# Kernel tuning notes

Measured on AMD Instinct MI355X. Metric: run time of the kernel, lower is better.

The kernel has to match this reference:

```python
import jax, jax.numpy as jnp
import numpy as np
from jax.ops import segment_sum, segment_max

B = 512          # parcels (batch of graphs)
P = 200          # poi nodes per parcel
N = B * P        # total poi nodes
E_POI = N * 16   # intra-parcel poi graph edges
HID = 256
IN_CH = 64
HEADS = 3
OUT = 12
T0 = 0.9
SLOPE = 0.2      # GATConv leaky_relu negative slope
NODE_GRAPH = jnp.arange(N, dtype=jnp.int32) // P  # poi node -> parcel id
ARANGE_N = jnp.arange(N, dtype=jnp.int32)


def setup_inputs() -> dict:
    key = jax.random.key(0)
    ks = jax.random.split(key, 24)
    g = lambda i, shape: jax.random.normal(ks[i], shape, jnp.float32) * 0.05
    # poi graph edges constrained within each parcel block
    src0 = jax.random.randint(ks[0], (E_POI,), 0, N, dtype=jnp.int32)
    off = jax.random.randint(ks[1], (E_POI,), 0, P, dtype=jnp.int32)
    return dict(
        g_poi_features=jax.random.normal(ks[2], (N, IN_CH), jnp.float32),
        img_feat=jax.random.normal(ks[3], (B, 2048), jnp.float32),
        edge_src=src0,
        edge_dst=(src0 // P) * P + off,
        W_gcn1=g(4, (IN_CH, HID)), b_gcn1=jnp.zeros((HID,), jnp.float32),
        W_gcn2=g(5, (HID, HID)), b_gcn2=jnp.zeros((HID,), jnp.float32),
        W_hrs=g(6, (2048, HID)), b_hrs=jnp.zeros((HID,), jnp.float32),
        W_proj_hrs=g(7, (HID, HID)), b_proj_hrs=jnp.zeros((HID,), jnp.float32),
        W_proj_poi=g(8, (HID, HID)), b_proj_poi=jnp.zeros((HID,), jnp.float32),
        W_gat_in=g(9, (HID, HEADS * HID)), al_in=g(10, (HEADS, HID)), ar_in=g(11, (HEADS, HID)),
        W_gat_with=g(12, (HID, HEADS * HID)), al_with=g(13, (HEADS, HID)), ar_with=g(14, (HEADS, HID)),
        W_hrsgnn=g(15, (HID, HID)),
        W_poignn=g(16, (HID, HID)),
        W_fc=g(17, (4 * HID, OUT)), b_fc=jnp.zeros((OUT,), jnp.float32),
    )


def _gcn(x, src, dst, W, b):
    # DGL GraphConv, norm='both', self-loops added
    s = jnp.concatenate([src, ARANGE_N])
    d = jnp.concatenate([dst, ARANGE_N])
    deg = segment_sum(jnp.ones_like(s, jnp.float32), d, num_segments=N)
    norm = jax.lax.rsqrt(jnp.maximum(deg, 1.0))
    h = (x @ W) * norm[:, None]
    m = segment_sum(h[s], d, num_segments=N)
    return m * norm[:, None] + b


def _gat(h_src, h_dst, src, dst, n_dst, W, al, ar):
    # DGL GATConv math: shared fc, additive attention, edge-softmax over dst
    fs = (h_src @ W).reshape(-1, HEADS, HID)
    fd = (h_dst @ W).reshape(-1, HEADS, HID)
    el = (fs * al).sum(-1)   # [n_src, H]
    er = (fd * ar).sum(-1)   # [n_dst, H]
    e = el[src] + er[dst]
    e = jnp.where(e > 0, e, SLOPE * e)
    m = segment_max(e, dst, num_segments=n_dst)
    w = jnp.exp(e - m[dst])
    z = segment_sum(w, dst, num_segments=n_dst)
    alpha = w / (z[dst] + 1e-9)
    out = segment_sum(fs[src] * alpha[:, :, None], dst, num_segments=n_dst)
    return out.mean(1)  # mean over heads (parcel_output.mean(1) in source)


def _mean_nodes(x):
    # dgl.mean_nodes over uniform-size batched graphs
    return segment_sum(x, NODE_GRAPH, num_segments=B) / P


def reference(g_poi_features, img_feat, edge_src, edge_dst,
              W_gcn1, b_gcn1, W_gcn2, b_gcn2, W_hrs, b_hrs,
              W_proj_hrs, b_proj_hrs, W_proj_poi, b_proj_poi,
              W_gat_in, al_in, ar_in, W_gat_with, al_with, ar_with,
              W_hrsgnn, W_poignn, W_fc, b_fc):
    # hrs_encoder: ResNet50 backbone modeled as precomputed 2048-d feats + replaced fc
    hrs = img_feat @ W_hrs + b_hrs                                  # [B, HID]
    # poi_encoder: 2-layer GCN over batched poi graph
    x = jax.nn.relu(_gcn(g_poi_features, edge_src, edge_dst, W_gcn1, b_gcn1))
    poi_nodes = _gcn(x, edge_src, edge_dst, W_gcn2, b_gcn2)         # [N, HID]
    poi_pooled = _mean_nodes(poi_nodes)                             # [B, HID]
    # mid-level fused similarity
    med = jnp.concatenate([hrs, poi_pooled], axis=1)
    med = med / jnp.linalg.norm(med, axis=1, keepdims=True)
    med_output = (med @ med.T + 1.0) / 2.0                          # [B, B]
    # UniSimGraph: GCN on thresholded parcel-similarity graph
    adj = jnp.where(med_output >= T0, 1.0, 0.0)
    adj = jnp.maximum(adj, jnp.eye(B, dtype=jnp.float32))
    dinv = jax.lax.rsqrt(adj.sum(1))
    nadj = adj * dinv[:, None] * dinv[None, :]
    hrs_agg = jax.nn.relu(nadj @ (hrs @ W_hrsgnn))                  # [B, HID]
    poi_agg = jax.nn.relu(nadj @ (poi_pooled @ W_poignn))           # [B, HID]
    # getHetGraph: bipartite poi<->parcel GAT, 3 heads, sum-aggregate, head-mean
    ph = hrs @ W_proj_hrs + b_proj_hrs                              # parcel feats
    pp = poi_nodes @ W_proj_poi + b_proj_poi                        # poi feats
    poi2img = _gat(pp, ph, ARANGE_N, NODE_GRAPH, B, W_gat_in, al_in, ar_in)      # [B, HID]
    img2poi = _gat(ph, pp, NODE_GRAPH, ARANGE_N, N, W_gat_with, al_with, ar_with)  # [N, HID]
    img2poi_pooled = _mean_nodes(img2poi)                           # [B, HID]
    # MutualAgg concat order: [img2poi, poi2poi(=poi_agg), poi2img, img2img(=hrs_agg)]
    agg = jnp.concatenate([img2poi_pooled, poi_agg, poi2img, hrs_agg], axis=1)
    output = agg @ W_fc + b_fc                                      # [B, OUT]
    return (output, med_output)
```

## Files before the change

kernel.cpp:

```cpp
#include <hip/hip_runtime.h>
#include <hip/hip_bf16.h>
#include <math.h>


#define N_NODES 102400
#define B_PAR   512
#define P_NODES 200
#define E_EDGES 1638400
#define HIDF    256

typedef __attribute__((ext_vector_type(8))) short bf16x8;
typedef __attribute__((ext_vector_type(4))) float f32x4;

__device__ __forceinline__ unsigned short f2bf(float x) {
    unsigned u = __builtin_bit_cast(unsigned, x);
    u += 0x7fffu + ((u >> 16) & 1u);
    return (unsigned short)(u >> 16);
}
__device__ __forceinline__ float bf2f(unsigned short h) {
    return __builtin_bit_cast(float, (unsigned)h << 16);
}
__device__ __forceinline__ int lds_off(int row, int kbyte) {
    return row * 128 + ((((kbyte >> 4) ^ (row & 7)) << 4) | (kbyte & 15));
}
template<bool BF16SRC>
__device__ __forceinline__ bf16x8 load_row8(const void* p, size_t elemoff) {
    if constexpr (BF16SRC) {
        return *(const bf16x8*)((const unsigned short*)p + elemoff);
    } else {
        const float* ap = (const float*)p + elemoff;
        float4 lo = *(const float4*)ap;
        float4 hi = *(const float4*)(ap + 4);
        union { bf16x8 v; unsigned short u[8]; } pk;
        pk.u[0] = f2bf(lo.x); pk.u[1] = f2bf(lo.y);
        pk.u[2] = f2bf(lo.z); pk.u[3] = f2bf(lo.w);
        pk.u[4] = f2bf(hi.x); pk.u[5] = f2bf(hi.y);
        pk.u[6] = f2bf(hi.z); pk.u[7] = f2bf(hi.w);
        return pk.v;
    }
}
__device__ __forceinline__ bf16x8 u8x8_to_bf16(uint2 w) {
    union { bf16x8 v; unsigned short u[8]; } r;
#pragma unroll
    for (int b = 0; b < 4; ++b) {
        r.u[b]     = (unsigned short)(__builtin_bit_cast(unsigned,
                        (float)((w.x >> (8 * b)) & 255u)) >> 16);
        r.u[4 + b] = (unsigned short)(__builtin_bit_cast(unsigned,
                        (float)((w.y >> (8 * b)) & 255u)) >> 16);
    }
    return r.v;
}
__device__ __forceinline__ unsigned long long pack4bf(f32x4 v) {
    union { unsigned long long u; unsigned short h[4]; } pk;
    pk.h[0] = f2bf(v[0]); pk.h[1] = f2bf(v[1]);
    pk.h[2] = f2bf(v[2]); pk.h[3] = f2bf(v[3]);
    return pk.u;
}

__global__ __launch_bounds__(512, 2) void gcnA_k(
    const unsigned char* __restrict__ Adj, const float* __restrict__ gp,
    const float* __restrict__ nrm, const unsigned short* __restrict__ W1t,
    const float* __restrict__ b1, unsigned short* __restrict__ X1nT)
{
    __shared__ unsigned char XnU[32768];
    __shared__ unsigned char AXU[32768];

    const int tid  = threadIdx.x;
    const int p    = blockIdx.x;
    const int lane = tid & 63;
    const int wave = tid >> 6;
    const int frow = lane & 15;
    const int fq   = lane >> 4;
    const int r4   = fq << 2;
    const f32x4 fz = {0.f, 0.f, 0.f, 0.f};

    uint2 adjr[2][7];
#pragma unroll
    for (int mi = 0; mi < 2; ++mi) {
        const unsigned char* ar = Adj + ((size_t)p << 16)
            + (size_t)(wave * 32 + mi * 16 + frow) * 256 + fq * 8;
#pragma unroll
        for (int ks = 0; ks < 7; ++ks)
            adjr[mi][ks] = *(const uint2*)(ar + ks * 32);
    }
    bf16x8 w1f[2][2];
#pragma unroll
    for (int mi = 0; mi < 2; ++mi)
#pragma unroll
        for (int ks = 0; ks < 2; ++ks)
            w1f[mi][ks] = *(const bf16x8*)(W1t
                + (size_t)(wave * 32 + mi * 16 + frow) * 64 + ks * 32 + fq * 8);

    for (int gi = wave; gi < 28; gi += 8) {
        int s0 = gi * 8;
        union { bf16x8 v; unsigned short h[8]; } pk;
#pragma unroll
        for (int t = 0; t < 8; ++t) {
            int s = s0 + t;
            float val = 0.f;
            if (s < 200)
                val = gp[((size_t)(p * 200 + s)) * 64 + lane] * nrm[p * 200 + s];
            pk.h[t] = f2bf(val);
        }
        *(bf16x8*)(XnU + lds_off((s0 >> 6) * 64 + lane, (s0 & 63) * 2)) = pk.v;
    }
    __syncthreads();

#pragma unroll
    for (int mi_d = 0; mi_d < 2; ++mi_d) {
        bf16x8 adjf[7];
#pragma unroll
        for (int ks = 0; ks < 7; ++ks) adjf[ks] = u8x8_to_bf16(adjr[mi_d][ks]);
#pragma unroll
        for (int kt = 0; kt < 4; ++kt) {
            f32x4 a2 = fz;
#pragma unroll
            for (int ks = 0; ks < 7; ++ks) {
                bf16x8 af = *(const bf16x8*)(XnU + lds_off(
                    (ks >> 1) * 64 + kt * 16 + frow, ((ks & 1) * 32 + fq * 8) * 2));
                a2 = __builtin_amdgcn_mfma_f32_16x16x32_bf16(af, adjf[ks], a2, 0, 0, 0);
            }
            *(unsigned long long*)(AXU + lds_off(
                wave * 32 + mi_d * 16 + frow, kt * 32 + fq * 8)) = pack4bf(a2);
        }
    }
    __syncthreads();

    f32x4 acc3[2][16];
#pragma unroll
    for (int i = 0; i < 2; ++i)
#pragma unroll
        for (int j = 0; j < 16; ++j) acc3[i][j] = fz;
#pragma unroll
    for (int ks = 0; ks < 2; ++ks)
#pragma unroll
        for (int ni = 0; ni < 16; ++ni) {
            bf16x8 bfr = *(const bf16x8*)(AXU + lds_off(
                ni * 16 + frow, ks * 64 + fq * 16));
            acc3[0][ni] = __builtin_amdgcn_mfma_f32_16x16x32_bf16(w1f[0][ks], bfr, acc3[0][ni], 0, 0, 0);
            acc3[1][ni] = __builtin_amdgcn_mfma_f32_16x16x32_bf16(w1f[1][ks], bfr, acc3[1][ni], 0, 0, 0);
        }

    float nrd[16];
#pragma unroll
    for (int ni = 0; ni < 16; ++ni) {
        int d = ni * 16 + frow;
        nrd[ni] = (d < 200) ? nrm[p * 200 + d] : 0.f;
    }
#pragma unroll
    for (int mi = 0; mi < 2; ++mi)
#pragma unroll
        for (int j = 0; j < 4; ++j) {
            int f = wave * 32 + mi * 16 + r4 + j;
            float bv = b1[f];
#pragma unroll
            for (int ni = 0; ni < 16; ++ni) {
                int d = ni * 16 + frow;
                if (d < 224) {
                    float v = fmaxf(acc3[mi][ni][j] * nrd[ni] + bv, 0.f) * nrd[ni];
                    X1nT[((size_t)p * 256 + f) * 224 + d] = f2bf(v);
                }
            }
        }
}

__global__ __launch_bounds__(512, 2) void gcnBG_k(
    const unsigned char* __restrict__ Adj, const unsigned short* __restrict__ X1nT,
    const unsigned short* __restrict__ W2t, const float* __restrict__ nrm,
    const float* __restrict__ b2, const float* __restrict__ er,
    const float* __restrict__ wu, float* __restrict__ qout,
    float* __restrict__ pool, unsigned short* __restrict__ poolb)
{
    __shared__ unsigned char BbU[2][16384];
    __shared__ unsigned char AXbU[16384];
    __shared__ unsigned char W2bU[16384];
    __shared__ float wush[768];
    __shared__ float esh[600];
    __shared__ float qsh[1024];
    __shared__ float mz[8];

    const int tid  = threadIdx.x;
    const int p    = blockIdx.x;
    const int lane = tid & 63;
    const int wave = tid >> 6;
    const int frow = lane & 15;
    const int fq   = lane >> 4;
    const int r4   = fq << 2;
    const f32x4 fz = {0.f, 0.f, 0.f, 0.f};

    bf16x8 adjb[2][7];
#pragma unroll
    for (int mi = 0; mi < 2; ++mi) {
        const unsigned char* ar = Adj + ((size_t)p << 16)
            + (size_t)(wave * 32 + mi * 16 + frow) * 256 + fq * 8;
#pragma unroll
        for (int ks = 0; ks < 7; ++ks)
            adjb[mi][ks] = u8x8_to_bf16(*(const uint2*)(ar + ks * 32));
    }

    for (int i = tid; i < 768; i += 512) wush[i] = wu[i];
    for (int i = tid; i < 1024; i += 512) qsh[i] = 0.f;

    f32x4 acc5[2][16];
#pragma unroll
    for (int i = 0; i < 2; ++i)
#pragma unroll
        for (int j = 0; j < 16; ++j) acc5[i][j] = fz;

    auto bbDst = [&](unsigned char* base, int idx) {
        int fl = idx / 28, soct = idx - fl * 28;
        int s0 = soct * 8;
        return base + lds_off((s0 >> 6) * 32 + fl, (s0 & 63) * 2);
    };
    auto bbSrc = [&](int c, int idx) {
        int fl = idx / 28, soct = idx - fl * 28;
        return (const uint4*)(X1nT + ((size_t)p * 256 + c * 32 + fl) * 224 + soct * 8);
    };
    auto w2Dst = [&](int idx) {
        int f = idx >> 2, oct = idx & 3;
        return W2bU + lds_off(f >> 1, (f & 1) * 64 + oct * 16);
    };

    {
        *(uint4*)bbDst(BbU[0], tid) = *bbSrc(0, tid);
        if (tid < 384) *(uint4*)bbDst(BbU[0], tid + 512) = *bbSrc(0, tid + 512);
#pragma unroll
        for (int i = 0; i < 2; ++i) {
            int idx = tid + i * 512;
            int f = idx >> 2, oct = idx & 3;
            *(uint4*)w2Dst(idx) = *(const uint4*)(W2t + (size_t)f * 256 + oct * 8);
        }
    }
    __syncthreads();

    uint4 stw[2];
    for (int c = 0; c < 8; ++c) {
        if (c > 0) {
#pragma unroll
            for (int i = 0; i < 2; ++i)
                *(uint4*)w2Dst(tid + i * 512) = stw[i];
        }
        uint4 stb0, stb1;
        if (c < 7) {
            stb0 = *bbSrc(c + 1, tid);
            if (tid < 384) stb1 = *bbSrc(c + 1, tid + 512);
#pragma unroll
            for (int i = 0; i < 2; ++i) {
                int idx = tid + i * 512;
                int f = idx >> 2, oct = idx & 3;
                stw[i] = *(const uint4*)(W2t + (size_t)f * 256 + (c + 1) * 32 + oct * 8);
            }
        }
        const unsigned char* Bc = BbU[c & 1];
        f32x4 acc4[2][2];
#pragma unroll
        for (int i = 0; i < 2; ++i)
#pragma unroll
            for (int j = 0; j < 2; ++j) acc4[i][j] = fz;
#pragma unroll
        for (int ks = 0; ks < 7; ++ks) {
#pragma unroll
            for (int mi_f = 0; mi_f < 2; ++mi_f) {
                bf16x8 af = *(const bf16x8*)(Bc + lds_off(
                    (ks >> 1) * 32 + mi_f * 16 + frow, ((ks & 1) * 32 + fq * 8) * 2));
                acc4[0][mi_f] = __builtin_amdgcn_mfma_f32_16x16x32_bf16(af, adjb[0][ks], acc4[0][mi_f], 0, 0, 0);
                acc4[1][mi_f] = __builtin_amdgcn_mfma_f32_16x16x32_bf16(af, adjb[1][ks], acc4[1][mi_f], 0, 0, 0);
            }
        }
#pragma unroll
        for (int mi_d = 0; mi_d < 2; ++mi_d)
#pragma unroll
            for (int mi_f = 0; mi_f < 2; ++mi_f)
                *(unsigned long long*)(AXbU + lds_off(
                    wave * 16 + mi_d * 8 + (frow >> 1),
                    (frow & 1) * 64 + mi_f * 32 + fq * 8))
                    = pack4bf(acc4[mi_d][mi_f]);
        __syncthreads();
        bf16x8 a5[2];
        a5[0] = *(const bf16x8*)(AXbU + lds_off(
            wave * 16 + (frow >> 1), (frow & 1) * 64 + fq * 16));
        a5[1] = *(const bf16x8*)(AXbU + lds_off(
            wave * 16 + 8 + (frow >> 1), (frow & 1) * 64 + fq * 16));
#pragma unroll
        for (int ni = 0; ni < 16; ++ni) {
            bf16x8 bfr = *(const bf16x8*)(W2bU + lds_off(
                ni * 8 + (frow >> 1), (frow & 1) * 64 + fq * 16));
            acc5[0][ni] = __builtin_amdgcn_mfma_f32_16x16x32_bf16(a5[0], bfr, acc5[0][ni], 0, 0, 0);
            acc5[1][ni] = __builtin_amdgcn_mfma_f32_16x16x32_bf16(a5[1], bfr, acc5[1][ni], 0, 0, 0);
        }
        if (c < 7) {
            *(uint4*)bbDst(BbU[(c + 1) & 1], tid) = stb0;
            if (tid < 384) *(uint4*)bbDst(BbU[(c + 1) & 1], tid + 512) = stb1;
        }
        __syncthreads();
    }

    float b2v[16], nrv[2][4];
#pragma unroll
    for (int ni = 0; ni < 16; ++ni) b2v[ni] = b2[ni * 16 + frow];
#pragma unroll
    for (int mi = 0; mi < 2; ++mi)
#pragma unroll
        for (int j = 0; j < 4; ++j) {
            int d = wave * 32 + mi * 16 + r4 + j;
            nrv[mi][j] = (d < 200) ? nrm[p * 200 + d] : 0.f;
        }
    float er3[3];
#pragma unroll
    for (int h = 0; h < 3; ++h) er3[h] = er[p * 3 + h];

#pragma unroll
    for (int mi = 0; mi < 2; ++mi)
#pragma unroll
        for (int j = 0; j < 4; ++j) {
            float e0 = 0.f, e1 = 0.f, e2 = 0.f;
            float nr = nrv[mi][j];
#pragma unroll
            for (int ni = 0; ni < 16; ++ni) {
                float vv = acc5[mi][ni][j] * nr + b2v[ni];
                int wb = (ni * 16 + frow) * 3;
                e0 += vv * wush[wb];
                e1 += vv * wush[wb + 1];
                e2 += vv * wush[wb + 2];
            }
#pragma unroll
            for (int o = 1; o < 16; o <<= 1) {
                e0 += __shfl_xor(e0, o);
                e1 += __shfl_xor(e1, o);
                e2 += __shfl_xor(e2, o);
            }
            int d = wave * 32 + mi * 16 + r4 + j;
            if (frow == 0 && d < 200) {
                float t0 = e0 + er3[0]; t0 = t0 > 0.f ? t0 : 0.2f * t0;
                float t1 = e1 + er3[1]; t1 = t1 > 0.f ? t1 : 0.2f * t1;
                float t2 = e2 + er3[2]; t2 = t2 > 0.f ? t2 : 0.2f * t2;
                esh[d * 3 + 0] = t0;
                esh[d * 3 + 1] = t1;
                esh[d * 3 + 2] = t2;
            }
        }
    __syncthreads();

    if (wave < 3) {
        float mx = -1e30f;
        for (int n = lane; n < 200; n += 64) mx = fmaxf(mx, esh[n * 3 + wave]);
#pragma unroll
        for (int o = 32; o > 0; o >>= 1) mx = fmaxf(mx, __shfl_xor(mx, o));
        float sm = 0.f;
        for (int n = lane; n < 200; n += 64) sm += expf(esh[n * 3 + wave] - mx);
#pragma unroll
        for (int o = 32; o > 0; o >>= 1) sm += __shfl_xor(sm, o);
        if (lane == 0) { mz[wave] = mx; mz[4 + wave] = sm; }
    }
    __syncthreads();

    float alph[2][4][3];
#pragma unroll
    for (int mi = 0; mi < 2; ++mi)
#pragma unroll
        for (int j = 0; j < 4; ++j) {
            int d = wave * 32 + mi * 16 + r4 + j;
#pragma unroll
            for (int h = 0; h < 3; ++h)
                alph[mi][j][h] = (d < 200)
                    ? expf(esh[d * 3 + h] - mz[h]) / (mz[4 + h] + 1e-9f) : 0.f;
        }

#pragma unroll
    for (int cfn = 0; cfn < 4; ++cfn) {
        float qacc[16];
#pragma unroll
        for (int ni = 0; ni < 16; ++ni) qacc[ni] = 0.f;
        float csum = 0.f;
#pragma unroll
        for (int mi = 0; mi < 2; ++mi)
#pragma unroll
            for (int j = 0; j < 4; ++j) {
                int d = wave * 32 + mi * 16 + r4 + j;
                float coef = 0.f;
                if (d < 200) coef = (cfn < 3) ? alph[mi][j][cfn] : 0.005f;
                float cn = coef * nrv[mi][j];
                csum += coef;
#pragma unroll
                for (int ni = 0; ni < 16; ++ni)
                    qacc[ni] += cn * acc5[mi][ni][j];
            }
#pragma unroll
        for (int ni = 0; ni < 16; ++ni) {
            float v = qacc[ni] + csum * b2v[ni];
            v += __shfl_xor(v, 16);
            v += __shfl_xor(v, 32);
            if (fq == 0) atomicAdd(&qsh[cfn * 256 + ni * 16 + frow], v);
        }
    }
    __syncthreads();

    for (int i = tid; i < 1024; i += 512) {
        int cfn = i >> 8, f = i & 255;
        float s = qsh[i];
        if (cfn < 3) {
            qout[(size_t)p * 768 + i] = s;
        } else {
            pool[(size_t)p * 256 + f] = s;
            poolb[(size_t)p * 256 + f] = f2bf(s);
        }
    }
}

template<bool ABF16, bool BBF16, int OMODE, bool BIASF, bool RELUF,
         bool MEDOUT, int KCHUNK>
__global__ __launch_bounds__(256) void mm64_k(
    const void* __restrict__ Ain, const void* __restrict__ Bin,
    void* __restrict__ Cout, int M, int Nc, int K,
    const float* __restrict__ bias, float alpha)
{
    __shared__ bf16x8 smem_v[1024];
    unsigned char* Asm = (unsigned char*)smem_v;
    unsigned char* Bsm = Asm + 8192;

    const int tid  = threadIdx.x;
    const int m0   = blockIdx.y * 64;
    const int n0   = blockIdx.x * 64;
    const int sr   = tid >> 3, sc = tid & 7;
    const int lane = tid & 63;
    const int wm   = (tid >> 7) & 1, wn = (tid >> 6) & 1;
    const int frow = lane & 15;
    const int fko  = (lane >> 4) << 4;

    int kbeg = 0, kend = K;
    float* Cf = (float*)Cout;
    if (KCHUNK > 0) {
        kbeg = blockIdx.z * KCHUNK; kend = kbeg + KCHUNK;
        Cf += (size_t)blockIdx.z * M * Nc;
    }

    f32x4 acc[2][2];
    const f32x4 fz = {0.f, 0.f, 0.f, 0.f};
#pragma unroll
    for (int i = 0; i < 2; ++i)
#pragma unroll
        for (int j = 0; j < 2; ++j) acc[i][j] = fz;

    bf16x8 areg[2], breg[2];
    auto load_tiles = [&](int k0) {
#pragma unroll
        for (int i = 0; i < 2; ++i) {
            int row = sr + 32 * i;
            areg[i] = load_row8<ABF16>(Ain, (size_t)(m0 + row) * K + k0 + sc * 8);
            breg[i] = load_row8<BBF16>(Bin, (size_t)(n0 + row) * K + k0 + sc * 8);
        }
    };

    load_tiles(kbeg);
    for (int k0 = kbeg; k0 < kend; k0 += 64) {
        __syncthreads();
#pragma unroll
        for (int i = 0; i < 2; ++i) {
            *(bf16x8*)(Asm + lds_off(sr + 32 * i, sc * 16)) = areg[i];
            *(bf16x8*)(Bsm + lds_off(sr + 32 * i, sc * 16)) = breg[i];
        }
        __syncthreads();
        if (k0 + 64 < kend) load_tiles(k0 + 64);
#pragma unroll
        for (int ks = 0; ks < 2; ++ks) {
            const int kb = ks * 64 + fko;
            bf16x8 af[2], bfr[2];
#pragma unroll
            for (int t = 0; t < 2; ++t)
                af[t] = *(const bf16x8*)(Asm + lds_off(wm * 32 + t * 16 + frow, kb));
#pragma unroll
            for (int t = 0; t < 2; ++t)
                bfr[t] = *(const bf16x8*)(Bsm + lds_off(wn * 32 + t * 16 + frow, kb));
#pragma unroll
            for (int mi = 0; mi < 2; ++mi)
#pragma unroll
                for (int ni = 0; ni < 2; ++ni)
                    acc[mi][ni] = __builtin_amdgcn_mfma_f32_16x16x32_bf16(
                        af[mi], bfr[ni], acc[mi][ni], 0, 0, 0);
        }
    }

    const int r4 = (lane >> 4) << 2;
#pragma unroll
    for (int mi = 0; mi < 2; ++mi) {
#pragma unroll
        for (int ni = 0; ni < 2; ++ni) {
            int col = n0 + wn * 32 + ni * 16 + frow;
#pragma unroll
            for (int j = 0; j < 4; ++j) {
                int row = m0 + wm * 32 + mi * 16 + r4 + j;
                float v = acc[mi][ni][j] * alpha;
                if (BIASF)  v += bias[col];
                if (RELUF)  v = fmaxf(v, 0.f);
                if (MEDOUT) v += 0.5f;
                if (OMODE == 0) {
                    Cf[(size_t)row * Nc + col] = v;
                } else {
                    ((unsigned short*)Cout)[(size_t)row * Nc + col] = f2bf(v);
                }
            }
        }
    }
}

__global__ __launch_bounds__(256) void edge_diag_k(
    const int* __restrict__ esrc, const int* __restrict__ edst,
    unsigned char* __restrict__ A)
{
    int id = blockIdx.x * 256 + threadIdx.x;
    size_t bo;
    if (id < E_EDGES) {
        int s = esrc[id], d = edst[id];
        int p = d / 200;
        int dl = d - p * 200, sl = s - p * 200;
        bo = (((size_t)(p * 256 + dl)) << 8) + (unsigned)sl;
    } else {
        int i2 = id - E_EDGES;
        int p = i2 / 200, d = i2 - p * 200;
        bo = (((size_t)(p * 256 + d)) << 8) + (unsigned)d;
    }
    atomicAdd((unsigned int*)(A + (bo & ~(size_t)3)), 1u << ((bo & 3) * 8));
}

__global__ __launch_bounds__(256) void norm2_k(const unsigned char* __restrict__ A,
                                               float* __restrict__ nrm)
{
    int g = blockIdx.x * 256 + threadIdx.x;
    int p = g / 200, d = g - p * 200;
    const uint4* row = (const uint4*)(A + (((size_t)(p * 256 + d)) << 8));
    unsigned s = 0;
#pragma unroll
    for (int i = 0; i < 16; ++i) {
        uint4 w = row[i];
        unsigned a = w.x, b = w.y, c = w.z, e = w.w;
        s += (a & 255) + ((a >> 8) & 255) + ((a >> 16) & 255) + (a >> 24);
        s += (b & 255) + ((b >> 8) & 255) + ((b >> 16) & 255) + (b >> 24);
        s += (c & 255) + ((c >> 8) & 255) + ((c >> 16) & 255) + (c >> 24);
        s += (e & 255) + ((e >> 8) & 255) + ((e >> 16) & 255) + (e >> 24);
    }
    nrm[g] = rsqrtf((float)s);
}

__global__ __launch_bounds__(256) void prep_k(
    const float* __restrict__ W1, const float* __restrict__ W2,
    const float* __restrict__ Whg,
    const float* __restrict__ Wpg, const float* __restrict__ Whrs,
    const float* __restrict__ Wgin, const float* __restrict__ Wgw,
    const float* __restrict__ Wph, const float* __restrict__ img,
    unsigned short* __restrict__ W1t, unsigned short* __restrict__ W2t,
    unsigned short* __restrict__ Whgt,
    unsigned short* __restrict__ Wpgt, unsigned short* __restrict__ Whrst,
    unsigned short* __restrict__ Wgint, unsigned short* __restrict__ Wmt,
    unsigned short* __restrict__ Wphb, unsigned short* __restrict__ imgb)
{
// ... 113 lines not shown
        nadjb[(size_t)i * 512 + j] = f2bf(a * di * dinv[j]);
    }
}

__global__ __launch_bounds__(256) void uv1_k(
    const float* __restrict__ Wgin, const float* __restrict__ al,
    const float* __restrict__ ar,
    float* __restrict__ u2, float* __restrict__ v2)
{
    const int wave = threadIdx.x >> 6, lane = threadIdx.x & 63;
    const int task = blockIdx.x * 4 + wave;
    const int k = task / 3, h = task - k * 3;
    float4 w = *(const float4*)(Wgin + (size_t)k * 768 + h * 256 + lane * 4);
    float4 a = *(const float4*)(al + h * 256 + lane * 4);
    float4 r = *(const float4*)(ar + h * 256 + lane * 4);
    float su = w.x * a.x + w.y * a.y + w.z * a.z + w.w * a.w;
    float sv = w.x * r.x + w.y * r.y + w.z * r.z + w.w * r.w;
#pragma unroll
    for (int o = 32; o > 0; o >>= 1) {
        su += __shfl_xor(su, o);
        sv += __shfl_xor(sv, o);
    }
    if (lane == 0) { u2[task] = su; v2[task] = sv; }
}

__global__ __launch_bounds__(256) void uv2_k(
    const float* __restrict__ Wph, const float* __restrict__ Wpp,
    const float* __restrict__ bph, const float* __restrict__ bpp,
    const unsigned short* __restrict__ Wmt,
    const float* __restrict__ u2, const float* __restrict__ v2,
    float* __restrict__ vv2, float* __restrict__ wu,
    float* __restrict__ bc, float* __restrict__ erb, float* __restrict__ eb0)
{
    __shared__ float ush[768], vsh[768];
    const int tid = threadIdx.x;
    for (int i = tid; i < 768; i += 256) { ush[i] = u2[i]; vsh[i] = v2[i]; }
    __syncthreads();
    const int wave = tid >> 6, lane = tid & 63;
    const int task = blockIdx.x * 4 + wave;
    float s = 0.f;
    if (task < 1536) {
        int t2 = task < 768 ? task : task - 768;
        int k = t2 / 3, h = t2 - k * 3;
        const float* W = task < 768 ? Wph : Wpp;
        const float* vec = task < 768 ? vsh : ush;
        float4 w = *(const float4*)(W + (size_t)k * 256 + lane * 4);
        s = w.x * vec[(lane * 4 + 0) * 3 + h] + w.y * vec[(lane * 4 + 1) * 3 + h]
          + w.z * vec[(lane * 4 + 2) * 3 + h] + w.w * vec[(lane * 4 + 3) * 3 + h];
#pragma unroll
        for (int o = 32; o > 0; o >>= 1) s += __shfl_xor(s, o);
        if (lane == 0) { if (task < 768) vv2[t2] = s; else wu[t2] = s; }
    } else if (task < 1792) {
        int k = task - 1536;
        float4 b4 = *(const float4*)(bph + lane * 4);
        const unsigned short* wm = Wmt + (size_t)k * 256 + lane * 4;
        s = b4.x * bf2f(wm[0]) + b4.y * bf2f(wm[1])
          + b4.z * bf2f(wm[2]) + b4.w * bf2f(wm[3]);
#pragma unroll
        for (int o = 32; o > 0; o >>= 1) s += __shfl_xor(s, o);
        if (lane == 0) bc[k] = s;
    } else if (task < 1798) {
        int t2 = task - 1792;
        int h = t2 % 3;
        bool second = t2 >= 3;
        const float* bias = second ? bpp : bph;
        const float* vec  = second ? ush : vsh;
        float4 b4 = *(const float4*)(bias + lane * 4);
        s = b4.x * vec[(lane * 4 + 0) * 3 + h] + b4.y * vec[(lane * 4 + 1) * 3 + h]
          + b4.z * vec[(lane * 4 + 2) * 3 + h] + b4.w * vec[(lane * 4 + 3) * 3 + h];
#pragma unroll
        for (int o = 32; o > 0; o >>= 1) s += __shfl_xor(s, o);
        if (lane == 0) { if (second) eb0[h] = s; else erb[h] = s; }
    }
}

__global__ __launch_bounds__(256) void er2_k(
    const float* __restrict__ hrs, const float* __restrict__ vv2,
    const float* __restrict__ erb, const float* __restrict__ eb0,
    float* __restrict__ er)
{
    __shared__ float vsh[768];
    const int tid = threadIdx.x;
    for (int i = tid; i < 768; i += 256) vsh[i] = vv2[i];
    __syncthreads();
    const int wave = tid >> 6, lane = tid & 63;
    const int task = blockIdx.x * 4 + wave;
    const int b = task / 3, h = task - b * 3;
    float4 hv = *(const float4*)(hrs + (size_t)b * 256 + lane * 4);
    float s = hv.x * vsh[(lane * 4 + 0) * 3 + h] + hv.y * vsh[(lane * 4 + 1) * 3 + h]
            + hv.z * vsh[(lane * 4 + 2) * 3 + h] + hv.w * vsh[(lane * 4 + 3) * 3 + h];
#pragma unroll
    for (int o = 32; o > 0; o >>= 1) s += __shfl_xor(s, o);
    if (lane == 0) er[task] = erb[h] + eb0[h] + s;
}

__global__ __launch_bounds__(256) void final_k(
    const float* __restrict__ i2p, const float* __restrict__ hpagg,
    const float* __restrict__ p2i,
    const float* __restrict__ Wfc, const float* __restrict__ bfc,
    float* __restrict__ out)
{
    int id = blockIdx.x * 256 + threadIdx.x;
    if (id >= B_PAR * 12) return;
    int b = id / 12, o = id % 12;
    float acc = bfc[o];
    const float* s0 = i2p + (size_t)b * 256;
    const float* s1 = hpagg + (size_t)b * 512 + 256;
    const float* s2 = p2i + (size_t)b * 256;
    const float* s3 = hpagg + (size_t)b * 512;
    for (int k = 0; k < 256; ++k) {
        acc += s0[k] * Wfc[(size_t)(0 * 256 + k) * 12 + o];
        acc += s1[k] * Wfc[(size_t)(1 * 256 + k) * 12 + o];
        acc += s2[k] * Wfc[(size_t)(2 * 256 + k) * 12 + o];
        acc += s3[k] * Wfc[(size_t)(3 * 256 + k) * 12 + o];
    }
    out[id] = acc;
}

extern "C" void kernel_launch(void* const* d_in, const int* in_sizes, int n_in,
                              void* d_out, int out_size, void* d_ws, size_t ws_size,
                              hipStream_t stream)
{
    const float* g_poi = (const float*)d_in[0];
    const float* img   = (const float*)d_in[1];
    const int*   esrc  = (const int*)d_in[2];
    const int*   edst  = (const int*)d_in[3];
    const float* W1    = (const float*)d_in[4];
    const float* b1    = (const float*)d_in[5];
    const float* W2    = (const float*)d_in[6];
    const float* b2    = (const float*)d_in[7];
    const float* Whrs  = (const float*)d_in[8];
    const float* bhrs  = (const float*)d_in[9];
    const float* Wph   = (const float*)d_in[10];
    const float* bph   = (const float*)d_in[11];
    const float* Wpp   = (const float*)d_in[12];
    const float* bpp   = (const float*)d_in[13];
    const float* Wgin  = (const float*)d_in[14];
    const float* alin  = (const float*)d_in[15];
    const float* arin  = (const float*)d_in[16];
    const float* Wgw   = (const float*)d_in[17];
    const float* Whg   = (const float*)d_in[20];
    const float* Wpg   = (const float*)d_in[21];
    const float* Wfc   = (const float*)d_in[22];
    const float* bfc   = (const float*)d_in[23];

    float* out     = (float*)d_out;
    float* med_out = out + B_PAR * 12;

    char* ws = (char*)d_ws;
    size_t off = 0;
    auto take = [&](size_t bytes) { void* pv = ws + off; off += (bytes + 255) & ~(size_t)255; return pv; };

    unsigned char*  adj8 = (unsigned char*)take((size_t)B_PAR * 256 * 256);
    unsigned short* X1nT = (unsigned short*)take((size_t)B_PAR * 256 * 224 * 2);
    float*          part = (float*)take((size_t)8 * 512 * 256 * 4);

    unsigned short* W1t   = (unsigned short*)take(256 * 64 * 2);
    unsigned short* W2t   = (unsigned short*)take(256 * 256 * 2);
    unsigned short* Whgt  = (unsigned short*)take(256 * 256 * 2);
    unsigned short* Wpgt  = (unsigned short*)take(256 * 256 * 2);
    unsigned short* Whrst = (unsigned short*)take((size_t)256 * 2048 * 2);
    unsigned short* Wgint = (unsigned short*)take((size_t)256 * 768 * 2);
    unsigned short* Wmt   = (unsigned short*)take(256 * 256 * 2);
    unsigned short* Wphb  = (unsigned short*)take(256 * 256 * 2);
    unsigned short* WcT   = (unsigned short*)take(256 * 256 * 2);
    unsigned short* WpG   = (unsigned short*)take((size_t)256 * 768 * 2);
    unsigned short* imgb  = (unsigned short*)take((size_t)512 * 2048 * 2);
    unsigned short* hrsb  = (unsigned short*)take((size_t)B_PAR * 256 * 2);
    unsigned short* poolb = (unsigned short*)take((size_t)B_PAR * 256 * 2);
    unsigned short* medb  = (unsigned short*)take((size_t)B_PAR * 512 * 2);
    unsigned short* nadjb = (unsigned short*)take((size_t)B_PAR * 512 * 2);
    unsigned short* Tcatt = (unsigned short*)take((size_t)512 * 512 * 2);
    float* nrm   = (float*)take((size_t)N_NODES * 4);
    float* hrs   = (float*)take((size_t)B_PAR * 256 * 4);
    float* pool  = (float*)take((size_t)B_PAR * 256 * 4);
    float* dinv  = (float*)take((size_t)B_PAR * 4);
    float* hpagg = (float*)take((size_t)B_PAR * 512 * 4);
    float* u2    = (float*)take(768 * 4);
    float* v2    = (float*)take(768 * 4);
    float* wu    = (float*)take(768 * 4);
    float* vv2   = (float*)take(768 * 4);
    float* erb   = (float*)take(16);
    float* eb0   = (float*)take(16);
    float* bc    = (float*)take(256 * 4);
    float* bgg   = (float*)take(256 * 4);
    float* er    = (float*)take((size_t)B_PAR * 3 * 4);
    float* q     = (float*)take((size_t)B_PAR * 768 * 4);
    float* p2i   = (float*)take((size_t)B_PAR * 256 * 4);
    float* i2p   = (float*)take((size_t)B_PAR * 256 * 4);
    (void)ws_size; (void)in_sizes; (void)n_in; (void)out_size;

    hipMemsetAsync(adj8, 0, (size_t)B_PAR * 256 * 256, stream);
    prep_k<<<8256, 256, 0, stream>>>(W1, W2, Whg, Wpg, Whrs, Wgin, Wgw,
        Wph, img, W1t, W2t, Whgt, Wpgt, Whrst, Wgint, Wmt, Wphb, imgb);
    edge_diag_k<<<(E_EDGES + N_NODES) / 256, 256, 0, stream>>>(esrc, edst, adj8);
    norm2_k<<<N_NODES / 256, 256, 0, stream>>>(adj8, nrm);
    wpg_k<<<769, 256, 0, stream>>>(Wpp, Wgin, bpp, WpG, bgg);

    mm64_k<true, true, 0, false, false, false, 256>
        <<<dim3(4, 8, 8), 256, 0, stream>>>(imgb, Whrst, part, 512, 256, 2048,
            nullptr, 1.f);
    hrs_reduce_k<<<512, 256, 0, stream>>>(part, bhrs, hrs, hrsb);

    uv1_k<<<192, 256, 0, stream>>>(Wgin, alin, arin, u2, v2);
    uv2_k<<<450, 256, 0, stream>>>(Wph, Wpp, bph, bpp, Wmt, u2, v2,
                                   vv2, wu, bc, erb, eb0);
    er2_k<<<384, 256, 0, stream>>>(hrs, vv2, erb, eb0, er);
    mm64_k<true, true, 1, false, false, false, 0>
        <<<dim3(4, 4), 256, 0, stream>>>(Wmt, Wphb, WcT, 256, 256, 256,
            nullptr, 1.f);

    gcnA_k<<<B_PAR, 512, 0, stream>>>(adj8, g_poi, nrm, W1t, b1, X1nT);
    gcnBG_k<<<B_PAR, 512, 0, stream>>>(adj8, X1nT, W2t, nrm, b2, er, wu,
                                       q, pool, poolb);

    med_build_k<<<B_PAR, 256, 0, stream>>>(hrs, pool, medb);
    mm64_k<true, true, 0, false, false, true, 0>
        <<<dim3(8, 8), 256, 0, stream>>>(medb, medb, med_out, 512, 512, 512,
            nullptr, 0.5f);

    dinv_k<<<B_PAR, 256, 0, stream>>>(med_out, dinv);
    nadj_k<<<B_PAR, 256, 0, stream>>>(med_out, dinv, nadjb);
    mm64_k<true, true, 1, false, false, false, 0>
        <<<dim3(8, 4), 256, 0, stream>>>(Whgt, hrsb, Tcatt, 256, 512, 256,
            nullptr, 1.f);
    mm64_k<true, true, 1, false, false, false, 0>
        <<<dim3(8, 4), 256, 0, stream>>>(Wpgt, poolb, Tcatt + (size_t)256 * 512,
            256, 512, 256, nullptr, 1.f);
    mm64_k<true, true, 0, false, true, false, 0>
        <<<dim3(8, 8), 256, 0, stream>>>(nadjb, Tcatt, hpagg, 512, 512, 512,
            nullptr, 1.f);

    mm64_k<false, true, 0, true, false, false, 0>
        <<<dim3(4, 8), 256, 0, stream>>>(q, WpG, p2i, 512, 256, 768,
            bgg, 1.f / 3.f);

    mm64_k<true, true, 0, true, false, false, 0>
        <<<dim3(4, 8), 256, 0, stream>>>(hrsb, WcT, i2p, 512, 256, 256,
            bc, 1.f);

    final_k<<<24, 256, 0, stream>>>(i2p, hpagg, p2i, Wfc, bfc, out);
}
```

Baseline: 376.0 us.

## Fuse the two GCN layer kernels into one block-per-parcel kernel

```diff
diff --git a/kernel.cpp b/kernel.cpp
--- a/kernel.cpp
+++ b/kernel.cpp
@@ -57,13 +57,25 @@
     return pk.u;
 }
 
-__global__ __launch_bounds__(512, 2) void gcnA_k(
+__global__ __launch_bounds__(1024, 1) void gcnF_k(
     const unsigned char* __restrict__ Adj, const float* __restrict__ gp,
     const float* __restrict__ nrm, const unsigned short* __restrict__ W1t,
-    const float* __restrict__ b1, unsigned short* __restrict__ X1nT)
-{
-    __shared__ unsigned char XnU[32768];
-    __shared__ unsigned char AXU[32768];
+    const float* __restrict__ b1, const unsigned short* __restrict__ W2t,
+    const float* __restrict__ b2, const float* __restrict__ er,
+    const float* __restrict__ wu, float* __restrict__ qout,
+    float* __restrict__ pool, unsigned short* __restrict__ poolb)
+{
+    __shared__ unsigned char lds[151552];
+    unsigned short* X1  = (unsigned short*)lds;
+    unsigned char*  SCR = lds + 118784;
+    unsigned short* XnT = (unsigned short*)SCR;
+    unsigned char*  AX1 = SCR;
+    unsigned char*  AXb = SCR;
+    unsigned char*  W2b = SCR + 16384;
+    float* wushF = (float*)SCR;
+    float* eshF  = (float*)(SCR + 4096);
+    float* qshF  = (float*)(SCR + 8192);
+    float* mzF   = (float*)(SCR + 12544);
 
     const int tid  = threadIdx.x;
     const int p    = blockIdx.x;
@@ -71,27 +83,22 @@
     const int wave = tid >> 6;
     const int frow = lane & 15;
     const int fq   = lane >> 4;
-    const int r4   = fq << 2;
     const f32x4 fz = {0.f, 0.f, 0.f, 0.f};
 
-    uint2 adjr[2][7];
-#pragma unroll
-    for (int mi = 0; mi < 2; ++mi) {
+    uint2 adjr[7];
+    {
         const unsigned char* ar = Adj + ((size_t)p << 16)
-            + (size_t)(wave * 32 + mi * 16 + frow) * 256 + fq * 8;
-#pragma unroll
-        for (int ks = 0; ks < 7; ++ks)
-            adjr[mi][ks] = *(const uint2*)(ar + ks * 32);
-    }
-    bf16x8 w1f[2][2];
-#pragma unroll
-    for (int mi = 0; mi < 2; ++mi)
-#pragma unroll
-        for (int ks = 0; ks < 2; ++ks)
-            w1f[mi][ks] = *(const bf16x8*)(W1t
-                + (size_t)(wave * 32 + mi * 16 + frow) * 64 + ks * 32 + fq * 8);
-
-    for (int gi = wave; gi < 28; gi += 8) {
+            + (size_t)(wave * 16 + frow) * 256 + fq * 8;
+#pragma unroll
+        for (int ks = 0; ks < 7; ++ks) adjr[ks] = *(const uint2*)(ar + ks * 32);
+    }
+    bf16x8 w1f[2];
+#pragma unroll
+    for (int ks = 0; ks < 2; ++ks)
+        w1f[ks] = *(const bf16x8*)(W1t
+            + (size_t)(wave * 16 + frow) * 64 + ks * 32 + fq * 8);
+
+    for (int gi = wave; gi < 28; gi += 16) {
         int s0 = gi * 8;
         union { bf16x8 v; unsigned short h[8]; } pk;
 #pragma unroll
@@ -102,269 +109,190 @@
                 val = gp[((size_t)(p * 200 + s)) * 64 + lane] * nrm[p * 200 + s];
             pk.h[t] = f2bf(val);
         }
-        *(bf16x8*)(XnU + lds_off((s0 >> 6) * 64 + lane, (s0 & 63) * 2)) = pk.v;
-    }
-    __syncthreads();
-
-#pragma unroll
-    for (int mi_d = 0; mi_d < 2; ++mi_d) {
+        *(bf16x8*)((unsigned char*)XnT + (size_t)lane * 464 + s0 * 2) = pk.v;
+    }
+    __syncthreads();
+
+    f32x4 acc2[4];
+#pragma unroll
+    for (int kt = 0; kt < 4; ++kt) acc2[kt] = fz;
+    {
         bf16x8 adjf[7];
 #pragma unroll
-        for (int ks = 0; ks < 7; ++ks) adjf[ks] = u8x8_to_bf16(adjr[mi_d][ks]);
-#pragma unroll
-        for (int kt = 0; kt < 4; ++kt) {
-            f32x4 a2 = fz;
-#pragma unroll
-            for (int ks = 0; ks < 7; ++ks) {
-                bf16x8 af = *(const bf16x8*)(XnU + lds_off(
-                    (ks >> 1) * 64 + kt * 16 + frow, ((ks & 1) * 32 + fq * 8) * 2));
-                a2 = __builtin_amdgcn_mfma_f32_16x16x32_bf16(af, adjf[ks], a2, 0, 0, 0);
+        for (int ks = 0; ks < 7; ++ks) adjf[ks] = u8x8_to_bf16(adjr[ks]);
+#pragma unroll
+        for (int ks = 0; ks < 7; ++ks)
+#pragma unroll
+            for (int kt = 0; kt < 4; ++kt) {
+                bf16x8 af = *(const bf16x8*)((unsigned char*)XnT
+                    + (size_t)(kt * 16 + frow) * 464 + (ks * 32 + fq * 8) * 2);
+                acc2[kt] = __builtin_amdgcn_mfma_f32_16x16x32_bf16(
+                    af, adjf[ks], acc2[kt], 0, 0, 0);
             }
-            *(unsigned long long*)(AXU + lds_off(
-                wave * 32 + mi_d * 16 + frow, kt * 32 + fq * 8)) = pack4bf(a2);
-        }
-    }
-    __syncthreads();
-
-    f32x4 acc3[2][16];
-#pragma unroll
-    for (int i = 0; i < 2; ++i)
-#pragma unroll
-        for (int j = 0; j < 16; ++j) acc3[i][j] = fz;
-#pragma unroll
-    for (int ks = 0; ks < 2; ++ks)
+    }
+    __syncthreads();
+#pragma unroll
+    for (int kt = 0; kt < 4; ++kt)
+        *(unsigned long long*)(AX1 + lds_off(
+            wave * 16 + frow, kt * 32 + fq * 8)) = pack4bf(acc2[kt]);
+    __syncthreads();
+
+    {
+        f32x4 acc3[16];
+#pragma unroll
+        for (int ni = 0; ni < 16; ++ni) acc3[ni] = fz;
+#pragma unroll
+        for (int ks = 0; ks < 2; ++ks)
+#pragma unroll
+            for (int ni = 0; ni < 16; ++ni) {
+                bf16x8 bfr = *(const bf16x8*)(AX1 + lds_off(
+                    ni * 16 + frow, ks * 64 + fq * 16));
+                acc3[ni] = __builtin_amdgcn_mfma_f32_16x16x32_bf16(
+                    w1f[ks], bfr, acc3[ni], 0, 0, 0);
+            }
+        float nrd[16];
 #pragma unroll
         for (int ni = 0; ni < 16; ++ni) {
-            bf16x8 bfr = *(const bf16x8*)(AXU + lds_off(
-                ni * 16 + frow, ks * 64 + fq * 16));
-            acc3[0][ni] = __builtin_amdgcn_mfma_f32_16x16x32_bf16(w1f[0][ks], bfr, acc3[0][ni], 0, 0, 0);
-            acc3[1][ni] = __builtin_amdgcn_mfma_f32_16x16x32_bf16(w1f[1][ks], bfr, acc3[1][ni], 0, 0, 0);
-        }
-
-    float nrd[16];
-#pragma unroll
-    for (int ni = 0; ni < 16; ++ni) {
-        int d = ni * 16 + frow;
-        nrd[ni] = (d < 200) ? nrm[p * 200 + d] : 0.f;
-    }
-#pragma unroll
-    for (int mi = 0; mi < 2; ++mi)
-#pragma unroll
-        for (int j = 0; j < 4; ++j) {
-            int f = wave * 32 + mi * 16 + r4 + j;
-            float bv = b1[f];
-#pragma unroll
-            for (int ni = 0; ni < 16; ++ni) {
-                int d = ni * 16 + frow;
-                if (d < 224) {
-                    float v = fmaxf(acc3[mi][ni][j] * nrd[ni] + bv, 0.f) * nrd[ni];
-                    X1nT[((size_t)p * 256 + f) * 224 + d] = f2bf(v);
+            int d = ni * 16 + frow;
+            nrd[ni] = (d < 200) ? nrm[p * 200 + d] : 0.f;
+        }
+        float b1v[4];
+#pragma unroll
+        for (int j = 0; j < 4; ++j) b1v[j] = b1[wave * 16 + fq * 4 + j];
+#pragma unroll
+        for (int ni = 0; ni < 16; ++ni) {
+            int d = ni * 16 + frow;
+            if (d < 224) {
+#pragma unroll
+                for (int j = 0; j < 4; ++j) {
+                    int f = wave * 16 + fq * 4 + j;
+                    float v = fmaxf(acc3[ni][j] * nrd[ni] + b1v[j], 0.f) * nrd[ni];
+                    X1[(size_t)f * 232 + d] = f2bf(v);
                 }
             }
         }
-}
-
-__global__ __launch_bounds__(512, 2) void gcnBG_k(
-    const unsigned char* __restrict__ Adj, const unsigned short* __restrict__ X1nT,
-    const unsigned short* __restrict__ W2t, const float* __restrict__ nrm,
-    const float* __restrict__ b2, const float* __restrict__ er,
-    const float* __restrict__ wu, float* __restrict__ qout,
-    float* __restrict__ pool, unsigned short* __restrict__ poolb)
-{
-    __shared__ unsigned char BbU[2][16384];
-    __shared__ unsigned char AXbU[16384];
-    __shared__ unsigned char W2bU[16384];
-    __shared__ float wush[768];
-    __shared__ float esh[600];
-    __shared__ float qsh[1024];
-    __shared__ float mz[8];
-
-    const int tid  = threadIdx.x;
-    const int p    = blockIdx.x;
-    const int lane = tid & 63;
-    const int wave = tid >> 6;
-    const int frow = lane & 15;
-    const int fq   = lane >> 4;
-    const int r4   = fq << 2;
-    const f32x4 fz = {0.f, 0.f, 0.f, 0.f};
-
-    bf16x8 adjb[2][7];
-#pragma unroll
-    for (int mi = 0; mi < 2; ++mi) {
-        const unsigned char* ar = Adj + ((size_t)p << 16)
-            + (size_t)(wave * 32 + mi * 16 + frow) * 256 + fq * 8;
-#pragma unroll
-        for (int ks = 0; ks < 7; ++ks)
-            adjb[mi][ks] = u8x8_to_bf16(*(const uint2*)(ar + ks * 32));
-    }
-
-    for (int i = tid; i < 768; i += 512) wush[i] = wu[i];
-    for (int i = tid; i < 1024; i += 512) qsh[i] = 0.f;
-
-    f32x4 acc5[2][16];
-#pragma unroll
-    for (int i = 0; i < 2; ++i)
-#pragma unroll
-        for (int j = 0; j < 16; ++j) acc5[i][j] = fz;
-
-    auto bbDst = [&](unsigned char* base, int idx) {
-        int fl = idx / 28, soct = idx - fl * 28;
-        int s0 = soct * 8;
-        return base + lds_off((s0 >> 6) * 32 + fl, (s0 & 63) * 2);
-    };
-    auto bbSrc = [&](int c, int idx) {
-        int fl = idx / 28, soct = idx - fl * 28;
-        return (const uint4*)(X1nT + ((size_t)p * 256 + c * 32 + fl) * 224 + soct * 8);
-    };
-    auto w2Dst = [&](int idx) {
-        int f = idx >> 2, oct = idx & 3;
-        return W2bU + lds_off(f >> 1, (f & 1) * 64 + oct * 16);
-    };
-
+    }
+    uint4 stw;
     {
-        *(uint4*)bbDst(BbU[0], tid) = *bbSrc(0, tid);
-        if (tid < 384) *(uint4*)bbDst(BbU[0], tid + 512) = *bbSrc(0, tid + 512);
-#pragma unroll
-        for (int i = 0; i < 2; ++i) {
-            int idx = tid + i * 512;
-            int f = idx >> 2, oct = idx & 3;
-            *(uint4*)w2Dst(idx) = *(const uint4*)(W2t + (size_t)f * 256 + oct * 8);
-        }
-    }
-    __syncthreads();
-
-    uint4 stw[2];
+        int f = tid >> 2, oct = tid & 3;
+        stw = *(const uint4*)(W2t + (size_t)f * 256 + oct * 8);
+    }
+    __syncthreads();
+
+    f32x4 acc5[16];
+#pragma unroll
+    for (int ni = 0; ni < 16; ++ni) acc5[ni] = fz;
+
     for (int c = 0; c < 8; ++c) {
-        if (c > 0) {
-#pragma unroll
-            for (int i = 0; i < 2; ++i)
-                *(uint4*)w2Dst(tid + i * 512) = stw[i];
-        }
-        uint4 stb0, stb1;
+        f32x4 acc4[2];
+        acc4[0] = fz; acc4[1] = fz;
+#pragma unroll
+        for (int ks = 0; ks < 7; ++ks) {
+            bf16x8 adjf = u8x8_to_bf16(adjr[ks]);
+#pragma unroll
+            for (int mi_f = 0; mi_f < 2; ++mi_f) {
+                bf16x8 af = *(const bf16x8*)((unsigned char*)X1
+                    + (size_t)(c * 32 + mi_f * 16 + frow) * 464
+                    + (ks * 32 + fq * 8) * 2);
+                acc4[mi_f] = __builtin_amdgcn_mfma_f32_16x16x32_bf16(
+                    af, adjf, acc4[mi_f], 0, 0, 0);
+            }
+        }
+#pragma unroll
+        for (int mi_f = 0; mi_f < 2; ++mi_f)
+            *(unsigned long long*)(AXb + lds_off(
+                wave * 8 + (frow >> 1),
+                (frow & 1) * 64 + mi_f * 32 + fq * 8)) = pack4bf(acc4[mi_f]);
+        {
+            int f = tid >> 2, oct = tid & 3;
+            *(uint4*)(W2b + lds_off(f >> 1, (f & 1) * 64 + oct * 16)) = stw;
+        }
+        __syncthreads();
         if (c < 7) {
-            stb0 = *bbSrc(c + 1, tid);
-            if (tid < 384) stb1 = *bbSrc(c + 1, tid + 512);
-#pragma unroll
-            for (int i = 0; i < 2; ++i) {
-                int idx = tid + i * 512;
-                int f = idx >> 2, oct = idx & 3;
-                stw[i] = *(const uint4*)(W2t + (size_t)f * 256 + (c + 1) * 32 + oct * 8);
-            }
-        }
-        const unsigned char* Bc = BbU[c & 1];
-        f32x4 acc4[2][2];
-#pragma unroll
-        for (int i = 0; i < 2; ++i)
-#pragma unroll
-            for (int j = 0; j < 2; ++j) acc4[i][j] = fz;
-#pragma unroll
-        for (int ks = 0; ks < 7; ++ks) {
-#pragma unroll
-            for (int mi_f = 0; mi_f < 2; ++mi_f) {
-                bf16x8 af = *(const bf16x8*)(Bc + lds_off(
-                    (ks >> 1) * 32 + mi_f * 16 + frow, ((ks & 1) * 32 + fq * 8) * 2));
-                acc4[0][mi_f] = __builtin_amdgcn_mfma_f32_16x16x32_bf16(af, adjb[0][ks], acc4[0][mi_f], 0, 0, 0);
-                acc4[1][mi_f] = __builtin_amdgcn_mfma_f32_16x16x32_bf16(af, adjb[1][ks], acc4[1][mi_f], 0, 0, 0);
-            }
-        }
-#pragma unroll
-        for (int mi_d = 0; mi_d < 2; ++mi_d)
-#pragma unroll
-            for (int mi_f = 0; mi_f < 2; ++mi_f)
-                *(unsigned long long*)(AXbU + lds_off(
-                    wave * 16 + mi_d * 8 + (frow >> 1),
-                    (frow & 1) * 64 + mi_f * 32 + fq * 8))
-                    = pack4bf(acc4[mi_d][mi_f]);
+            int f = tid >> 2, oct = tid & 3;
+            stw = *(const uint4*)(W2t + (size_t)f * 256 + (c + 1) * 32 + oct * 8);
+        }
+        bf16x8 a5 = *(const bf16x8*)(AXb + lds_off(
+            wave * 8 + (frow >> 1), (frow & 1) * 64 + fq * 16));
+#pragma unroll
+        for (int ni = 0; ni < 16; ++ni) {
+            int fp = ni * 16 + frow;
+            bf16x8 bfr = *(const bf16x8*)(W2b + lds_off(
+                fp >> 1, (fp & 1) * 64 + fq * 16));
+            acc5[ni] = __builtin_amdgcn_mfma_f32_16x16x32_bf16(
+                a5, bfr, acc5[ni], 0, 0, 0);
+        }
         __syncthreads();
-        bf16x8 a5[2];
-        a5[0] = *(const bf16x8*)(AXbU + lds_off(
-            wave * 16 + (frow >> 1), (frow & 1) * 64 + fq * 16));
-        a5[1] = *(const bf16x8*)(AXbU + lds_off(
-            wave * 16 + 8 + (frow >> 1), (frow & 1) * 64 + fq * 16));
+    }
+
+    if (tid < 768) wushF[tid] = wu[tid];
+    qshF[tid] = 0.f;
+    __syncthreads();
+
+    float b2v[16], nrv[4];
+#pragma unroll
+    for (int ni = 0; ni < 16; ++ni) b2v[ni] = b2[ni * 16 + frow];
+#pragma unroll
+    for (int j = 0; j < 4; ++j) {
+        int d = wave * 16 + fq * 4 + j;
+        nrv[j] = (d < 200) ? nrm[p * 200 + d] : 0.f;
+    }
+    float er3[3];
+#pragma unroll
+    for (int h = 0; h < 3; ++h) er3[h] = er[p * 3 + h];
+
+#pragma unroll
+    for (int j = 0; j < 4; ++j) {
+        float e0 = 0.f, e1 = 0.f, e2 = 0.f;
+        float nr = nrv[j];
 #pragma unroll
         for (int ni = 0; ni < 16; ++ni) {
-            bf16x8 bfr = *(const bf16x8*)(W2bU + lds_off(
-                ni * 8 + (frow >> 1), (frow & 1) * 64 + fq * 16));
-            acc5[0][ni] = __builtin_amdgcn_mfma_f32_16x16x32_bf16(a5[0], bfr, acc5[0][ni], 0, 0, 0);
-            acc5[1][ni] = __builtin_amdgcn_mfma_f32_16x16x32_bf16(a5[1], bfr, acc5[1][ni], 0, 0, 0);
-        }
-        if (c < 7) {
-            *(uint4*)bbDst(BbU[(c + 1) & 1], tid) = stb0;
-            if (tid < 384) *(uint4*)bbDst(BbU[(c + 1) & 1], tid + 512) = stb1;
-        }
-        __syncthreads();
-    }
-
-    float b2v[16], nrv[2][4];
-#pragma unroll
-    for (int ni = 0; ni < 16; ++ni) b2v[ni] = b2[ni * 16 + frow];
-#pragma unroll
-    for (int mi = 0; mi < 2; ++mi)
-#pragma unroll
-        for (int j = 0; j < 4; ++j) {
-            int d = wave * 32 + mi * 16 + r4 + j;
-            nrv[mi][j] = (d < 200) ? nrm[p * 200 + d] : 0.f;
-        }
-    float er3[3];
-#pragma unroll
-    for (int h = 0; h < 3; ++h) er3[h] = er[p * 3 + h];
-
-#pragma unroll
-    for (int mi = 0; mi < 2; ++mi)
-#pragma unroll
-        for (int j = 0; j < 4; ++j) {
-            float e0 = 0.f, e1 = 0.f, e2 = 0.f;
-            float nr = nrv[mi][j];
-#pragma unroll
-            for (int ni = 0; ni < 16; ++ni) {
-                float vv = acc5[mi][ni][j] * nr + b2v[ni];
-                int wb = (ni * 16 + frow) * 3;
-                e0 += vv * wush[wb];
-                e1 += vv * wush[wb + 1];
-                e2 += vv * wush[wb + 2];
-            }
-#pragma unroll
-            for (int o = 1; o < 16; o <<= 1) {
-                e0 += __shfl_xor(e0, o);
-                e1 += __shfl_xor(e1, o);
-                e2 += __shfl_xor(e2, o);
-            }
-            int d = wave * 32 + mi * 16 + r4 + j;
-            if (frow == 0 && d < 200) {
-                float t0 = e0 + er3[0]; t0 = t0 > 0.f ? t0 : 0.2f * t0;
-                float t1 = e1 + er3[1]; t1 = t1 > 0.f ? t1 : 0.2f * t1;
-                float t2 = e2 + er3[2]; t2 = t2 > 0.f ? t2 : 0.2f * t2;
-                esh[d * 3 + 0] = t0;
-                esh[d * 3 + 1] = t1;
-                esh[d * 3 + 2] = t2;
-            }
-        }
+            float vv = acc5[ni][j] * nr + b2v[ni];
+            int wb = (ni * 16 + frow) * 3;
+            e0 += vv * wushF[wb];
+            e1 += vv * wushF[wb + 1];
+            e2 += vv * wushF[wb + 2];
+        }
+#pragma unroll
+        for (int o = 1; o < 16; o <<= 1) {
+            e0 += __shfl_xor(e0, o);
+            e1 += __shfl_xor(e1, o);
+            e2 += __shfl_xor(e2, o);
+        }
+        int d = wave * 16 + fq * 4 + j;
+        if (frow == 0 && d < 200) {
+            float t0 = e0 + er3[0]; t0 = t0 > 0.f ? t0 : 0.2f * t0;
+            float t1 = e1 + er3[1]; t1 = t1 > 0.f ? t1 : 0.2f * t1;
+            float t2 = e2 + er3[2]; t2 = t2 > 0.f ? t2 : 0.2f * t2;
+            eshF[d * 3 + 0] = t0;
+            eshF[d * 3 + 1] = t1;
+            eshF[d * 3 + 2] = t2;
+        }
+    }
     __syncthreads();
 
     if (wave < 3) {
         float mx = -1e30f;
-        for (int n = lane; n < 200; n += 64) mx = fmaxf(mx, esh[n * 3 + wave]);
+        for (int n = lane; n < 200; n += 64) mx = fmaxf(mx, eshF[n * 3 + wave]);
 #pragma unroll
         for (int o = 32; o > 0; o >>= 1) mx = fmaxf(mx, __shfl_xor(mx, o));
         float sm = 0.f;
-        for (int n = lane; n < 200; n += 64) sm += expf(esh[n * 3 + wave] - mx);
+        for (int n = lane; n < 200; n += 64) sm += expf(eshF[n * 3 + wave] - mx);
 #pragma unroll
         for (int o = 32; o > 0; o >>= 1) sm += __shfl_xor(sm, o);
-        if (lane == 0) { mz[wave] = mx; mz[4 + wave] = sm; }
-    }
-    __syncthreads();
-
-    float alph[2][4][3];
-#pragma unroll
-    for (int mi = 0; mi < 2; ++mi)
-#pragma unroll
-        for (int j = 0; j < 4; ++j) {
-            int d = wave * 32 + mi * 16 + r4 + j;
-#pragma unroll
-            for (int h = 0; h < 3; ++h)
-                alph[mi][j][h] = (d < 200)
-                    ? expf(esh[d * 3 + h] - mz[h]) / (mz[4 + h] + 1e-9f) : 0.f;
-        }
+        if (lane == 0) { mzF[wave] = mx; mzF[4 + wave] = sm; }
+    }
+    __syncthreads();
+
+    float alph[4][3];
+#pragma unroll
+    for (int j = 0; j < 4; ++j) {
+        int d = wave * 16 + fq * 4 + j;
+#pragma unroll
+        for (int h = 0; h < 3; ++h)
+            alph[j][h] = (d < 200)
+                ? expf(eshF[d * 3 + h] - mzF[h]) / (mzF[4 + h] + 1e-9f) : 0.f;
+    }
 
 #pragma unroll
     for (int cfn = 0; cfn < 4; ++cfn) {
@@ -373,33 +301,31 @@
         for (int ni = 0; ni < 16; ++ni) qacc[ni] = 0.f;
         float csum = 0.f;
 #pragma unroll
-        for (int mi = 0; mi < 2; ++mi)
-#pragma unroll
-            for (int j = 0; j < 4; ++j) {
-                int d = wave * 32 + mi * 16 + r4 + j;
-                float coef = 0.f;
-                if (d < 200) coef = (cfn < 3) ? alph[mi][j][cfn] : 0.005f;
-                float cn = coef * nrv[mi][j];
-                csum += coef;
-#pragma unroll
-                for (int ni = 0; ni < 16; ++ni)
-                    qacc[ni] += cn * acc5[mi][ni][j];
-            }
+        for (int j = 0; j < 4; ++j) {
+            int d = wave * 16 + fq * 4 + j;
+            float coef = 0.f;
+            if (d < 200) coef = (cfn < 3) ? alph[j][cfn] : 0.005f;
+            float cn = coef * nrv[j];
+            csum += coef;
+#pragma unroll
+            for (int ni = 0; ni < 16; ++ni)
+                qacc[ni] += cn * acc5[ni][j];
+        }
 #pragma unroll
         for (int ni = 0; ni < 16; ++ni) {
             float v = qacc[ni] + csum * b2v[ni];
             v += __shfl_xor(v, 16);
             v += __shfl_xor(v, 32);
-            if (fq == 0) atomicAdd(&qsh[cfn * 256 + ni * 16 + frow], v);
-        }
-    }
-    __syncthreads();
-
-    for (int i = tid; i < 1024; i += 512) {
-        int cfn = i >> 8, f = i & 255;
-        float s = qsh[i];
+            if (fq == 0) atomicAdd(&qshF[cfn * 256 + ni * 16 + frow], v);
+        }
+    }
+    __syncthreads();
+
+    {
+        int cfn = tid >> 8, f = tid & 255;
+        float s = qshF[tid];
         if (cfn < 3) {
-            qout[(size_t)p * 768 + i] = s;
+            qout[(size_t)p * 768 + tid] = s;
         } else {
             pool[(size_t)p * 256 + f] = s;
             poolb[(size_t)p * 256 + f] = f2bf(s);
@@ -819,7 +745,6 @@
     auto take = [&](size_t bytes) { void* pv = ws + off; off += (bytes + 255) & ~(size_t)255; return pv; };
 
     unsigned char*  adj8 = (unsigned char*)take((size_t)B_PAR * 256 * 256);
-    unsigned short* X1nT = (unsigned short*)take((size_t)B_PAR * 256 * 224 * 2);
     float*          part = (float*)take((size_t)8 * 512 * 256 * 4);
 
     unsigned short* W1t   = (unsigned short*)take(256 * 64 * 2);
@@ -877,9 +802,8 @@
         <<<dim3(4, 4), 256, 0, stream>>>(Wmt, Wphb, WcT, 256, 256, 256,
             nullptr, 1.f);
 
-    gcnA_k<<<B_PAR, 512, 0, stream>>>(adj8, g_poi, nrm, W1t, b1, X1nT);
-    gcnBG_k<<<B_PAR, 512, 0, stream>>>(adj8, X1nT, W2t, nrm, b2, er, wu,
-                                       q, pool, poolb);
+    gcnF_k<<<B_PAR, 1024, 0, stream>>>(adj8, g_poi, nrm, W1t, b1, W2t, b2,
+                                       er, wu, q, pool, poolb);
 
     med_build_k<<<B_PAR, 256, 0, stream>>>(hrs, pool, medb);
     mm64_k<true, true, 0, false, false, true, 0>
```

Result: slower. 433.3 us (+15.3%).
